# Kernel tuning notes

Measured on AMD Instinct MI355X. Metric: run time of the kernel, lower is better.

Reference implementation:

```python
import jax, jax.numpy as jnp
import numpy as np
import math

STAGE_NUM = 5
EPS = 1e-6

def _l2norm(a, axis):
    return a / (EPS + jnp.linalg.norm(a, axis=axis, keepdims=True))

def setup_inputs() -> dict:
    key = jax.random.key(0)
    k1, k2, k3, k4 = jax.random.split(key, 4)
    b, n, c, h, w, k, out_c = 4, 4, 256, 64, 64, 128, 256
    x = jax.random.normal(k1, (b, c, h, w), dtype=jnp.float32)
    querys = jax.random.normal(k2, (b * n, c, h, w), dtype=jnp.float32)
    # mu init: normal(0, sqrt(2/k)) then l2norm over channel dim
    mu0 = jax.random.normal(k3, (1, c, k), dtype=jnp.float32) * math.sqrt(2.0 / k)
    mu0 = _l2norm(mu0, axis=1)
    # conv weight: normal(0, sqrt(2/(kh*kw*out_c)))
    fan = 3 * 3 * out_c
    conv_w = jax.random.normal(k4, (out_c, 2 * c, 3, 3), dtype=jnp.float32) * math.sqrt(2.0 / fan)
    conv_b = jnp.zeros((out_c,), dtype=jnp.float32)
    return {"x": x, "querys": querys, "mu0": mu0, "conv_w": conv_w, "conv_b": conv_b, "n": n}

def reference(x, querys, mu0, conv_w, conv_b, n):
    b, c, h, w = x.shape
    k = mu0.shape[2]
    xf = x.reshape(b, c, h * w)                       # [b, c, L]
    mu = jnp.broadcast_to(mu0, (b, c, k))

    # EM iterations (torch.no_grad -> stop_gradient)
    def em_step(mu, _):
        z = jnp.einsum('bcl,bck->blk', xf, mu)        # [b, L, k]
        z = jax.nn.softmax(z, axis=2)
        z_ = z / (EPS + jnp.sum(z, axis=1, keepdims=True))
        mu = jnp.einsum('bcl,blk->bck', xf, z_)       # [b, c, k]
        mu = _l2norm(mu, axis=1)
        return mu, None
    mu, _ = jax.lax.scan(em_step, mu, None, length=STAGE_NUM)
    mu = jax.lax.stop_gradient(mu)

    org_query = querys                                 # [b*n, c, h, w]
    q = querys.reshape(b, n, c, h, w).transpose(0, 2, 1, 3, 4).reshape(b, c, n * h * w)
    q_z = jax.nn.softmax(jnp.einsum('bcl,bck->blk', q, mu), axis=2)  # [b, nL, k]
    q_z = jax.lax.stop_gradient(q_z)

    rec = jnp.einsum('bck,blk->bcl', mu, q_z)          # [b, c, n*h*w]
    rec = rec.reshape(b, c, n, h, w).transpose(0, 2, 1, 3, 4).reshape(b * n, c, h, w)

    cat = jnp.concatenate((org_query, rec), axis=1)    # [b*n, 2c, h, w]
    out = jax.lax.conv_general_dilated(
        cat, conv_w, window_strides=(1, 1), padding='SAME',
        dimension_numbers=('NCHW', 'OIHW', 'NCHW'))
    out = out + conv_b[None, :, None, None]
    return (out, mu)
```

## Files before the change

### kernel.cpp

```cpp
#include <hip/hip_runtime.h>
#include <hip/hip_bf16.h>

#define B   4
#define NN  4
#define C   256
#define HH  64
#define WW  64
#define L   4096
#define NL  16384
#define K   128
#define OC  256
#define IC2 512
#define EPSV 1e-6f
#define PW  66
#define PA  4356

typedef __hip_bfloat16 bf16;
typedef __attribute__((ext_vector_type(8))) __bf16 bf16x8;
typedef __attribute__((ext_vector_type(4))) float f32x4;

#define AS1(p) ((const __attribute__((address_space(1))) void*)(p))
#define AS3(p) ((__attribute__((address_space(3))) void*)(p))

__global__ void k_init(const float* __restrict__ mu0, float* __restrict__ mu_f,
                       bf16* __restrict__ mub) {
    int i = blockIdx.x * 256 + threadIdx.x;
    int rem = i & 32767;
    int k = rem >> 8, c = rem & 255;
    float v = mu0[c * 128 + k];
    mu_f[i] = v;
    mub[i]  = __float2bfloat16(v);
}

__global__ void k_prepx(const float* __restrict__ x, bf16* __restrict__ xb,
                        bf16* __restrict__ xt) {
    __shared__ float ld[64][65];
    int lt = blockIdx.x, ct = blockIdx.y, b = blockIdx.z;
    int t = threadIdx.x;
    #pragma unroll
    for (int i = 0; i < 16; i++) {
        int idx = t + i * 256;
        int ch = idx >> 6, xl = idx & 63;
        size_t a = ((size_t)b * C + ct * 64 + ch) * L + lt * 64 + xl;
        float v = x[a];
        ld[ch][xl] = v;
        xb[a] = __float2bfloat16(v);
    }
    __syncthreads();
    #pragma unroll
    for (int i = 0; i < 16; i++) {
        int idx = t + i * 256;
        int xl = idx >> 6, ch = idx & 63;
        xt[((size_t)b * L + lt * 64 + xl) * 256 + ct * 64 + ch] = __float2bfloat16(ld[ch][xl]);
    }
}

__global__ void k_prepq(const float* __restrict__ qy, bf16* __restrict__ P2) {
    __shared__ float ld[64][65];
    int y = blockIdx.x, ct = blockIdx.y, img = blockIdx.z;
    int t = threadIdx.x;
    #pragma unroll
    for (int i = 0; i < 16; i++) {
        int idx = t + i * 256;
        int ch = idx >> 6, xl = idx & 63;
        ld[ch][xl] = qy[((size_t)img * C + ct * 64 + ch) * L + y * WW + xl];
    }
    __syncthreads();
    #pragma unroll
    for (int i = 0; i < 16; i++) {
        int idx = t + i * 256;
        int xl = idx >> 6, ch = idx & 63;
        P2[((size_t)img * PA + (size_t)(y + 1) * PW + xl + 1) * 512 + ct * 64 + ch] =
            __float2bfloat16(ld[ch][xl]);
    }
}

__global__ void k_zborder(uint4* __restrict__ P2) {
    int pi = blockIdx.x, img = blockIdx.y, t = threadIdx.x;
    int y, x;
    if      (pi < 66)  { y = 0;        x = pi; }
    else if (pi < 132) { y = 65;       x = pi - 66; }
    else if (pi < 196) { y = pi - 131; x = 0; }
    else               { y = pi - 195; x = 65; }
    P2[((size_t)img * PA + (size_t)y * PW + x) * 64 + t] = uint4{0, 0, 0, 0};
}

__global__ void k_wprep(const float* __restrict__ cw, bf16* __restrict__ wb) {
    int idx = blockIdx.x * 256 + threadIdx.x;
    if (idx >= 9 * OC * IC2) return;
    int r  = idx / (OC * IC2);
    int oc = (idx / IC2) & 255;
    int ic = idx & 511;
    wb[idx] = __float2bfloat16(cw[((size_t)oc * IC2 + ic) * 9 + r]);
}

__global__ void __launch_bounds__(256) k_z(const bf16* __restrict__ xt,
                                           const bf16* __restrict__ mub,
                                           bf16* __restrict__ zt) {
    __shared__ __align__(16) char smem[12288];
    char* tA = smem;
    char* tB = smem + 8192;
    int t = threadIdx.x, w = t >> 6, lane = t & 63;
    int b = blockIdx.y, l0 = blockIdx.x * 64;
    const bf16* Ab = mub + (size_t)b * K * C;
    const bf16* Bb = xt + ((size_t)b * L + l0) * C;
    int srow = t >> 2, sseg = t & 3, aseg = sseg ^ (srow & 3);
    char* dA0 = tA + w * 1024;
    char* dA1 = tA + 4096 + w * 1024;
    char* dB  = tB + w * 1024;
    int aoff[8], boff;
    #pragma unroll
    for (int i = 0; i < 8; i++) {
        int rowA = i * 16 + (lane & 15);
        aoff[i] = rowA * 64 + (((lane >> 4) ^ (rowA & 3)) << 4);
    }
    { int rowB = w * 16 + (lane & 15);
      boff = rowB * 64 + (((lane >> 4) ^ (rowB & 3)) << 4); }
    f32x4 acc[8];
    #pragma unroll
    for (int i = 0; i < 8; i++) acc[i] = f32x4{0.f, 0.f, 0.f, 0.f};
    for (int s = 0; s < 8; s++) {
        int cb0 = s * 32 + aseg * 8;
        __syncthreads();
        __builtin_amdgcn_global_load_lds(AS1(Ab + (size_t)srow * C + cb0),        AS3(dA0), 16, 0, 0);
        __builtin_amdgcn_global_load_lds(AS1(Ab + (size_t)(srow + 64) * C + cb0), AS3(dA1), 16, 0, 0);
        __builtin_amdgcn_global_load_lds(AS1(Bb + (size_t)srow * C + cb0),        AS3(dB),  16, 0, 0);
        __syncthreads();
        bf16x8 bfr = *(bf16x8*)(tB + boff);
        #pragma unroll
        for (int i = 0; i < 8; i++) {
            bf16x8 af = *(bf16x8*)(tA + aoff[i]);
            acc[i] = __builtin_amdgcn_mfma_f32_16x16x32_bf16(af, bfr, acc[i], 0, 0, 0);
        }
    }
    float m = -1e30f;
    #pragma unroll
    for (int i = 0; i < 8; i++)
        #pragma unroll
        for (int r = 0; r < 4; r++) m = fmaxf(m, acc[i][r]);
    m = fmaxf(m, __shfl_xor(m, 16, 64));
    m = fmaxf(m, __shfl_xor(m, 32, 64));
    float ssum = 0.f;
    #pragma unroll
    for (int i = 0; i < 8; i++)
        #pragma unroll
        for (int r = 0; r < 4; r++) { acc[i][r] = __expf(acc[i][r] - m); ssum += acc[i][r]; }
    ssum += __shfl_xor(ssum, 16, 64);
    ssum += __shfl_xor(ssum, 32, 64);
    float inv = 1.f / ssum;
    int quad = lane >> 4, col = lane & 15;
    bf16* zb = zt + (size_t)b * K * L + l0 + w * 16 + col;
    #pragma unroll
    for (int i = 0; i < 8; i++)
        #pragma unroll
        for (int r = 0; r < 4; r++) {
            int k = i * 16 + quad * 4 + r;
            zb[(size_t)k * L] = __float2bfloat16(acc[i][r] * inv);
        }
}

__global__ void __launch_bounds__(256) k_mu(const bf16* __restrict__ zt,
                                            const bf16* __restrict__ xb,
                                            float* __restrict__ part) {
    __shared__ __align__(16) char smem[12288];
    char* tA = smem;
    char* tB = smem + 8192;
    int t = threadIdx.x, w = t >> 6, lane = t & 63;
    int ct = blockIdx.x, chunk = blockIdx.y, b = blockIdx.z;
    const bf16* Ab = zt + (size_t)b * K * L + chunk * 256;
    const bf16* Bb = xb + ((size_t)b * C + ct * 64) * L + chunk * 256;
    int srow = t >> 2, sseg = t & 3, aseg = sseg ^ (srow & 3);
    char* dA0 = tA + w * 1024; char* dA1 = tA + 4096 + w * 1024;
    char* dB0 = tB + w * 1024;
    int wm = w >> 1, wn = w & 1;
    int aoff[4], boff[2];
    #pragma unroll
    for (int i = 0; i < 4; i++) {
        int rowA = wm * 64 + i * 16 + (lane & 15);
        aoff[i] = rowA * 64 + (((lane >> 4) ^ (rowA & 3)) << 4);
    }
    #pragma unroll
    for (int j = 0; j < 2; j++) {
        int rowB = wn * 32 + j * 16 + (lane & 15);
        boff[j] = rowB * 64 + (((lane >> 4) ^ (rowB & 3)) << 4);
    }
    f32x4 acc[4][2];
    #pragma unroll
    for (int i = 0; i < 4; i++)
        #pragma unroll
        for (int j = 0; j < 2; j++) acc[i][j] = f32x4{0.f, 0.f, 0.f, 0.f};
    for (int s = 0; s < 8; s++) {
        int lb = s * 32 + aseg * 8;
        __syncthreads();
        __builtin_amdgcn_global_load_lds(AS1(Ab + (size_t)srow * L + lb),        AS3(dA0), 16, 0, 0);
        __builtin_amdgcn_global_load_lds(AS1(Ab + (size_t)(srow + 64) * L + lb), AS3(dA1), 16, 0, 0);
        __builtin_amdgcn_global_load_lds(AS1(Bb + (size_t)srow * L + lb),        AS3(dB0), 16, 0, 0);
        __syncthreads();
        bf16x8 af[4], bfr[2];
        #pragma unroll
        for (int i = 0; i < 4; i++) af[i]  = *(bf16x8*)(tA + aoff[i]);
        #pragma unroll
        for (int j = 0; j < 2; j++) bfr[j] = *(bf16x8*)(tB + boff[j]);
        #pragma unroll
        for (int i = 0; i < 4; i++)
            #pragma unroll
            for (int j = 0; j < 2; j++)
                acc[i][j] = __builtin_amdgcn_mfma_f32_16x16x32_bf16(af[i], bfr[j], acc[i][j], 0, 0, 0);
    }
    float* pb = part + ((size_t)(b * 16 + chunk) * K) * C + ct * 64;
    int quad = lane >> 4, col = lane & 15;
    #pragma unroll
    for (int i = 0; i < 4; i++) {
        int k = wm * 64 + i * 16 + quad * 4;
        #pragma unroll
        for (int j = 0; j < 2; j++) {
            int c = wn * 32 + j * 16 + col;
            #pragma unroll
            for (int r = 0; r < 4; r++)
                pb[(size_t)(k + r) * C + c] = acc[i][j][r];
        }
    }
}

__global__ void k_norm(const float* __restrict__ part, float* __restrict__ mu_f,
                       bf16* __restrict__ mub, bf16* __restrict__ muT) {
    int b = blockIdx.x >> 7, k = blockIdx.x & 127, lane = threadIdx.x;
    float v[4] = {0.f, 0.f, 0.f, 0.f};
    for (int ch = 0; ch < 16; ch++) {
        const float* p = part + ((size_t)(b * 16 + ch) * K + k) * C;
        #pragma unroll
        for (int j = 0; j < 4; j++) v[j] += p[lane + j * 64];
    }
    float s = v[0]*v[0] + v[1]*v[1] + v[2]*v[2] + v[3]*v[3];
    for (int o = 32; o > 0; o >>= 1) s += __shfl_xor(s, o, 64);
    float r = 1.f / (EPSV + sqrtf(s));
    float* mf = mu_f + ((size_t)b * K + k) * C;
    bf16*  mb = mub  + ((size_t)b * K + k) * C;
    bf16*  mt = muT  + (size_t)b * C * K + k;
    #pragma unroll
    for (int j = 0; j < 4; j++) {
        float val = v[j] * r;
        int c = lane + j * 64;
        mf[c] = val;
        mb[c] = __float2bfloat16(val);
        mt[(size_t)c * K] = __float2bfloat16(val);
    }
}

__global__ void __launch_bounds__(256) k_qzrec(const bf16* __restrict__ P2r,
                                               const bf16* __restrict__ mub,
                                               const bf16* __restrict__ muT,
                                               bf16* __restrict__ P2w) {
    __shared__ __align__(16) char smem[46080];
    char* tA = smem;
    char* tB = smem + 4096;
    char* zl = smem + 12288;
    char* mt = smem + 29696;
    int t = threadIdx.x, w = t >> 6, lane = t & 63;
    int b = blockIdx.y, tile = blockIdx.x;
    int n = tile >> 6, y = tile & 63;
    int img = b * NN + n;
    const bf16* Ab = P2r + ((size_t)img * PA + (size_t)(y + 1) * PW + 1) * 512;
    const bf16* Bb = mub + (size_t)b * K * C;
    int srow = t >> 2, sseg = t & 3, aseg = sseg ^ (srow & 3);
    char* dA  = tA + w * 1024;
    char* dB0 = tB + w * 1024;
    char* dB1 = tB + 4096 + w * 1024;
    int q = lane >> 4, col = lane & 15;
    int boff[8], aoff;
    #pragma unroll
    for (int j = 0; j < 8; j++) {
        int rowB = j * 16 + col;
        boff[j] = rowB * 64 + ((q ^ (rowB & 3)) << 4);
    }
    { int rowA = w * 16 + col;
      aoff = rowA * 64 + ((q ^ (rowA & 3)) << 4); }
    f32x4 acc[8];
    #pragma unroll
    for (int j = 0; j < 8; j++) acc[j] = f32x4{0.f, 0.f, 0.f, 0.f};
    for (int s = 0; s < 8; s++) {
        int cb0 = s * 32 + aseg * 8;
        __syncthreads();
        __builtin_amdgcn_global_load_lds(AS1(Ab + (size_t)srow * 512 + cb0),      AS3(dA),  16, 0, 0);
        __builtin_amdgcn_global_load_lds(AS1(Bb + (size_t)srow * C + cb0),        AS3(dB0), 16, 0, 0);
        __builtin_amdgcn_global_load_lds(AS1(Bb + (size_t)(srow + 64) * C + cb0), AS3(dB1), 16, 0, 0);
        __syncthreads();
        bf16x8 af = *(bf16x8*)(tA + aoff);
        #pragma unroll
        for (int j = 0; j < 8; j++) {
            bf16x8 bfr = *(bf16x8*)(tB + boff[j]);
            acc[j] = __builtin_amdgcn_mfma_f32_16x16x32_bf16(af, bfr, acc[j], 0, 0, 0);
        }
    }
    #pragma unroll
    for (int r = 0; r < 4; r++) {
        float mm = acc[0][r];
        #pragma unroll
        for (int j = 1; j < 8; j++) mm = fmaxf(mm, acc[j][r]);
        mm = fmaxf(mm, __shfl_xor(mm, 1, 64));
        mm = fmaxf(mm, __shfl_xor(mm, 2, 64));
        mm = fmaxf(mm, __shfl_xor(mm, 4, 64));
        mm = fmaxf(mm, __shfl_xor(mm, 8, 64));
        float ss = 0.f;
        float e[8];
        #pragma unroll
        for (int j = 0; j < 8; j++) { e[j] = __expf(acc[j][r] - mm); ss += e[j]; }
        ss += __shfl_xor(ss, 1, 64);
        ss += __shfl_xor(ss, 2, 64);
        ss += __shfl_xor(ss, 4, 64);
        ss += __shfl_xor(ss, 8, 64);
        float inv = 1.f / ss;
        int zrow = w * 16 + q * 4 + r;
        #pragma unroll
        for (int j = 0; j < 8; j++)
            *(bf16*)(zl + zrow * 272 + (j * 16 + col) * 2) = __float2bfloat16(e[j] * inv);
    }
    const bf16* Mb = muT + (size_t)b * C * K;
    int mrow = (lane >> 2);
    int mseg = lane & 3;
    #pragma unroll
    for (int it2 = 0; it2 < 4; it2++) {
        int row = w * 64 + it2 * 16 + mrow;
        int sg = mseg ^ ((row ^ (row >> 2)) & 3);
        __builtin_amdgcn_global_load_lds(AS1(Mb + (size_t)row * K + sg * 8),
            AS3(mt + (w * 64 + it2 * 16) * 64), 16, 0, 0);
    }
    __syncthreads();
    bf16x8 afz[4];
    #pragma unroll
    for (int ch = 0; ch < 4; ch++)
        afz[ch] = *(bf16x8*)(zl + (w * 16 + col) * 272 + ch * 64 + q * 16);
    f32x4 acc2[16];
    #pragma unroll
    for (int j = 0; j < 16; j++) acc2[j] = f32x4{0.f, 0.f, 0.f, 0.f};
    for (int s = 0; s < 4; s++) {
        #pragma unroll
        for (int j = 0; j < 16; j++) {
            int rr = j * 16 + col;
            bf16x8 bm = *(bf16x8*)(mt + rr * 64 + ((q ^ ((rr ^ (rr >> 2)) & 3)) << 4));
            acc2[j] = __builtin_amdgcn_mfma_f32_16x16x32_bf16(afz[s], bm, acc2[j], 0, 0, 0);
        }
        if (s < 3) {
            __syncthreads();
            #pragma unroll
            for (int it2 = 0; it2 < 4; it2++) {
                int row = w * 64 + it2 * 16 + mrow;
                int sg = mseg ^ ((row ^ (row >> 2)) & 3);
                __builtin_amdgcn_global_load_lds(AS1(Mb + (size_t)row * K + (s + 1) * 32 + sg * 8),
                    AS3(mt + (w * 64 + it2 * 16) * 64), 16, 0, 0);
            }
            __syncthreads();
        }
    }
    #pragma unroll
    for (int r = 0; r < 4; r++) {
        int xg = w * 16 + q * 4 + r;
        bf16* dst = P2w + ((size_t)img * PA + (size_t)(y + 1) * PW + xg + 1) * 512 + 256;
        #pragma unroll
        for (int j = 0; j < 16; j++)
            dst[j * 16 + col] = __float2bfloat16(acc2[j][r]);
    }
}

__global__ void __launch_bounds__(256, 2) k_conv(const bf16* __restrict__ P2,
                                                 const bf16* __restrict__ Wb,
                                                 const float* __restrict__ cb,
                                                 float* __restrict__ out) {
    __shared__ __align__(16) char smem[49920];
    char* inl = smem;
    char* wld = smem + 25344;
    int t = threadIdx.x, w = t >> 6, lane = t & 63;
    int m0  = blockIdx.x * 128;
    int y0  = blockIdx.y * 4;
    int img = blockIdx.z;
    int srow = t >> 2;
    int aseg = (t & 3) ^ ((srow ^ (srow >> 2)) & 3);
    int wm = w >> 1, wn = w & 1;
    int q = lane >> 4, lane15 = lane & 15;

    int aoff[4];
    #pragma unroll
    for (int i = 0; i < 4; i++) {
        int rowA = wm * 64 + i * 16 + lane15;
        aoff[i] = rowA * 64 + (((q ^ (rowA ^ (rowA >> 2))) & 3) << 4);
    }

    auto stageIN = [&](int cc) {
        size_t ibase = (size_t)img * PA * 512 + cc * 32;
        #pragma unroll
        for (int it = 0; it < 6; it++) {
            unsigned g = it * 256 + t;
            unsigned row = g / 264u, ps = g - row * 264u;
            unsigned px = ps >> 2, s0 = ps & 3;
            unsigned sg = s0 ^ ((px ^ (px >> 1)) & 3);
            __builtin_amdgcn_global_load_lds(
                AS1(P2 + ibase + ((size_t)(y0 + row) * PW + px) * 512 + sg * 8),
                AS3(inl + it * 4096 + w * 1024), 16, 0, 0);
        }
        if (t < 48) {
            unsigned g = 1536 + t;
            unsigned row = g / 264u, ps = g - row * 264u;
            unsigned px = ps >> 2, s0 = ps & 3;
            unsigned sg = s0 ^ ((px ^ (px >> 1)) & 3);
            __builtin_amdgcn_global_load_lds(
                AS1(P2 + ibase + ((size_t)(y0 + row) * PW + px) * 512 + sg * 8),
                AS3(inl + 24576), 16, 0, 0);
        }
    };

    f32x4 acc[4][8];
    #pragma unroll
    for (int i = 0; i < 4; i++) {
        int oc = m0 + wm * 64 + i * 16 + q * 4;
        #pragma unroll
        for (int r = 0; r < 4; r++) {
            float bv = cb[oc + r];
            #pragma unroll
            for (int j = 0; j < 8; j++) acc[i][j][r] = bv;
        }
    }

    stageIN(0);
    {
        const bf16* w0 = Wb + (size_t)(m0 + srow) * IC2 + aseg * 8;
        __builtin_amdgcn_global_load_lds(AS1(w0),                         AS3(wld + w * 1024), 16, 0, 0);
        __builtin_amdgcn_global_load_lds(AS1(w0 + (size_t)64 * IC2),      AS3(wld + 4096 + w * 1024), 16, 0, 0);
        const bf16* w1 = w0 + (size_t)(OC * IC2);
        __builtin_amdgcn_global_load_lds(AS1(w1),                         AS3(wld + 8192 + w * 1024), 16, 0, 0);
        __builtin_amdgcn_global_load_lds(AS1(w1 + (size_t)64 * IC2),      AS3(wld + 8192 + 4096 + w * 1024), 16, 0, 0);
    }
    asm volatile("s_waitcnt vmcnt(0)" ::: "memory");
    __builtin_amdgcn_s_barrier();
    asm volatile("" ::: "memory");

    for (int cc = 0; cc < 16; cc++) {
        #pragma unroll
        for (int rt = 0; rt < 9; rt++) {
            const int dy = rt / 3, dx = rt % 3;
            char* wbuf = wld + (rt % 3) * 8192;
            bf16x8 af[4];
            #pragma unroll
            for (int i = 0; i < 4; i++) af[i] = *(bf16x8*)(wbuf + aoff[i]);
            const bool doPf = (cc * 9 + rt + 2) < 144;
            if (doPf) {
                const int g2 = rt + 2;
                const int rt2 = (g2 >= 9) ? g2 - 9 : g2;
                const int cc2 = cc + (g2 >= 9 ? 1 : 0);
                char* wdst = wld + ((rt + 2) % 3) * 8192;
                const bf16* wsrc = Wb + (size_t)rt2 * (OC * IC2) + (size_t)(m0 + srow) * IC2
                                 + cc2 * 32 + aseg * 8;
                __builtin_amdgcn_global_load_lds(AS1(wsrc),                    AS3(wdst + w * 1024), 16, 0, 0);
                __builtin_amdgcn_global_load_lds(AS1(wsrc + (size_t)64 * IC2), AS3(wdst + 4096 + w * 1024), 16, 0, 0);
            }
            __builtin_amdgcn_s_setprio(1);
            #pragma unroll
            for (int j = 0; j < 8; j++) {
                int p = (j & 3) * 16 + lane15 + dx;
                int rowsel = 2 * wn + (j >> 2) + dy;
                bf16x8 bfr = *(bf16x8*)(inl + rowsel * 4224 + p * 64 +
                                        (((q ^ (p ^ (p >> 1))) & 3) << 4));
                #pragma unroll
                for (int i = 0; i < 4; i++)
                    acc[i][j] = __builtin_amdgcn_mfma_f32_16x16x32_bf16(af[i], bfr, acc[i][j], 0, 0, 0);
            }
            __builtin_amdgcn_s_setprio(0);
            if (rt == 8) {
                if (cc < 15) {
                    asm volatile("" ::: "memory");
                    __builtin_amdgcn_s_barrier();
                    asm volatile("" ::: "memory");
                    stageIN(cc + 1);
                    asm volatile("s_waitcnt vmcnt(0)" ::: "memory");
                    __builtin_amdgcn_s_barrier();
                    asm volatile("" ::: "memory");
                }
            } else {
                if (doPf) asm volatile("s_waitcnt vmcnt(2)" ::: "memory");
                else      asm volatile("s_waitcnt vmcnt(0)" ::: "memory");
                __builtin_amdgcn_s_barrier();
                asm volatile("" ::: "memory");
            }
        }
    }

    #pragma unroll
    for (int i = 0; i < 4; i++) {
        int oc = m0 + wm * 64 + i * 16 + q * 4;
        #pragma unroll
        for (int j = 0; j < 8; j++) {
            int px = blockIdx.y * 256 + wn * 128 + (j >> 2) * 64 + (j & 3) * 16 + lane15;
            #pragma unroll
            for (int r = 0; r < 4; r++)
                out[((size_t)img * OC + oc + r) * L + px] = acc[i][j][r];
        }
    }
}

__global__ void k_muout(const float* __restrict__ mu_f, float* __restrict__ out) {
    int i = blockIdx.x * 256 + threadIdx.x;
    int b = i >> 15, rem = i & 32767;
    int c = rem >> 7, k = rem & 127;
    out[(size_t)16777216 + i] = mu_f[((size_t)b * K + k) * C + c];
}

extern "C" void kernel_launch(void* const* d_in, const int* in_sizes, int n_in,
                              void* d_out, int out_size, void* d_ws, size_t ws_size,
                              hipStream_t stream) {
    const float* x   = (const float*)d_in[0];
    const float* qy  = (const float*)d_in[1];
    const float* mu0 = (const float*)d_in[2];
    const float* cw  = (const float*)d_in[3];
    const float* cb  = (const float*)d_in[4];
    float* out = (float*)d_out;

    char* ws = (char*)d_ws;
    float* mu_f = (float*)(ws);
    bf16*  mu_b = (bf16*) (ws + 524288);
    bf16*  muT  = (bf16*) (ws + 786432);
    bf16*  Wb   = (bf16*) (ws + 1048576);
    bf16*  zt   = (bf16*) (ws + 3407872);
    bf16*  P2   = (bf16*) (ws + 20185088);
    bf16*  x_bf = (bf16*) (ws + 20185088);
    float* part = (float*)(ws + 20185088 + 8388608);
    bf16*  xt   = (bf16*) (ws + 20185088 + 16777216);

    k_init<<<512, 256, 0, stream>>>(mu0, mu_f, mu_b);
    k_prepx<<<dim3(64, 4, 4), 256, 0, stream>>>(x, x_bf, xt);

    for (int it = 0; it < 5; it++) {
        k_z<<<dim3(64, 4), 256, 0, stream>>>(xt, mu_b, zt);
        k_mu<<<dim3(4, 16, 4), 256, 0, stream>>>(zt, x_bf, part);
        k_norm<<<512, 64, 0, stream>>>(part, mu_f, mu_b, muT);
    }

    k_prepq<<<dim3(64, 4, 16), 256, 0, stream>>>(qy, P2);
    k_zborder<<<dim3(260, 16), 64, 0, stream>>>((uint4*)P2);
    k_wprep<<<4608, 256, 0, stream>>>(cw, Wb);

    k_qzrec<<<dim3(256, 4), 256, 0, stream>>>(P2, mu_b, muT, P2);
    k_conv<<<dim3(2, 16, 16), 256, 0, stream>>>(P2, Wb, cb, out);
    k_muout<<<512, 256, 0, stream>>>(mu_f, out);
}
```

Measured before the change: 405.3 us.

## Merge prep kernels, write mu output from norm, double-buffer muT staging in qzrec

```diff
diff --git a/kernel.cpp b/kernel.cpp
--- a/kernel.cpp
+++ b/kernel.cpp
@@ -22,14 +22,11 @@
 #define AS1(p) ((const __attribute__((address_space(1))) void*)(p))
 #define AS3(p) ((__attribute__((address_space(3))) void*)(p))
 
-__global__ void k_init(const float* __restrict__ mu0, float* __restrict__ mu_f,
-                       bf16* __restrict__ mub) {
+__global__ void k_init(const float* __restrict__ mu0, bf16* __restrict__ mub) {
     int i = blockIdx.x * 256 + threadIdx.x;
     int rem = i & 32767;
     int k = rem >> 8, c = rem & 255;
-    float v = mu0[c * 128 + k];
-    mu_f[i] = v;
-    mub[i]  = __float2bfloat16(v);
+    mub[i] = __float2bfloat16(mu0[c * 128 + k]);
 }
 
 __global__ void k_prepx(const float* __restrict__ x, bf16* __restrict__ xb,
@@ -55,43 +52,43 @@
     }
 }
 
-__global__ void k_prepq(const float* __restrict__ qy, bf16* __restrict__ P2) {
+__global__ void k_mid(const float* __restrict__ qy, bf16* __restrict__ P2,
+                      const float* __restrict__ cw, bf16* __restrict__ wb) {
     __shared__ float ld[64][65];
-    int y = blockIdx.x, ct = blockIdx.y, img = blockIdx.z;
-    int t = threadIdx.x;
-    #pragma unroll
-    for (int i = 0; i < 16; i++) {
-        int idx = t + i * 256;
-        int ch = idx >> 6, xl = idx & 63;
-        ld[ch][xl] = qy[((size_t)img * C + ct * 64 + ch) * L + y * WW + xl];
-    }
-    __syncthreads();
-    #pragma unroll
-    for (int i = 0; i < 16; i++) {
-        int idx = t + i * 256;
-        int xl = idx >> 6, ch = idx & 63;
-        P2[((size_t)img * PA + (size_t)(y + 1) * PW + xl + 1) * 512 + ct * 64 + ch] =
-            __float2bfloat16(ld[ch][xl]);
-    }
-}
-
-__global__ void k_zborder(uint4* __restrict__ P2) {
-    int pi = blockIdx.x, img = blockIdx.y, t = threadIdx.x;
-    int y, x;
-    if      (pi < 66)  { y = 0;        x = pi; }
-    else if (pi < 132) { y = 65;       x = pi - 66; }
-    else if (pi < 196) { y = pi - 131; x = 0; }
-    else               { y = pi - 195; x = 65; }
-    P2[((size_t)img * PA + (size_t)y * PW + x) * 64 + t] = uint4{0, 0, 0, 0};
-}
-
-__global__ void k_wprep(const float* __restrict__ cw, bf16* __restrict__ wb) {
-    int idx = blockIdx.x * 256 + threadIdx.x;
-    if (idx >= 9 * OC * IC2) return;
-    int r  = idx / (OC * IC2);
-    int oc = (idx / IC2) & 255;
-    int ic = idx & 511;
-    wb[idx] = __float2bfloat16(cw[((size_t)oc * IC2 + ic) * 9 + r]);
+    int bid = blockIdx.x, t = threadIdx.x;
+    if (bid < 4096) {
+        int y = bid & 63, ct = (bid >> 6) & 3, img = bid >> 8;
+        #pragma unroll
+        for (int i = 0; i < 16; i++) {
+            int idx = t + i * 256;
+            int ch = idx >> 6, xl = idx & 63;
+            ld[ch][xl] = qy[((size_t)img * C + ct * 64 + ch) * L + y * WW + xl];
+        }
+        __syncthreads();
+        #pragma unroll
+        for (int i = 0; i < 16; i++) {
+            int idx = t + i * 256;
+            int xl = idx >> 6, ch = idx & 63;
+            P2[((size_t)img * PA + (size_t)(y + 1) * PW + xl + 1) * 512 + ct * 64 + ch] =
+                __float2bfloat16(ld[ch][xl]);
+        }
+    } else if (bid < 5136) {
+        int zi = bid - 4096;
+        int img = zi / 65, grp = zi - img * 65;
+        int pi = grp * 4 + (t >> 6), tt = t & 63;
+        int y, x;
+        if      (pi < 66)  { y = 0;        x = pi; }
+        else if (pi < 132) { y = 65;       x = pi - 66; }
+        else if (pi < 196) { y = pi - 131; x = 0; }
+        else               { y = pi - 195; x = 65; }
+        ((uint4*)P2)[((size_t)img * PA + (size_t)y * PW + x) * 64 + tt] = uint4{0, 0, 0, 0};
+    } else {
+        int idx = (bid - 5136) * 256 + t;
+        int r  = idx / (OC * IC2);
+        int oc = (idx / IC2) & 255;
+        int ic = idx & 511;
+        wb[idx] = __float2bfloat16(cw[((size_t)oc * IC2 + ic) * 9 + r]);
+    }
 }
 
 __global__ void __launch_bounds__(256) k_z(const bf16* __restrict__ xt,
@@ -222,8 +219,8 @@
     }
 }
 
-__global__ void k_norm(const float* __restrict__ part, float* __restrict__ mu_f,
-                       bf16* __restrict__ mub, bf16* __restrict__ muT) {
+__global__ void k_norm(const float* __restrict__ part, bf16* __restrict__ mub,
+                       bf16* __restrict__ muT, float* __restrict__ outT, int last) {
     int b = blockIdx.x >> 7, k = blockIdx.x & 127, lane = threadIdx.x;
     float v[4] = {0.f, 0.f, 0.f, 0.f};
     for (int ch = 0; ch < 16; ch++) {
@@ -234,16 +231,15 @@
     float s = v[0]*v[0] + v[1]*v[1] + v[2]*v[2] + v[3]*v[3];
     for (int o = 32; o > 0; o >>= 1) s += __shfl_xor(s, o, 64);
     float r = 1.f / (EPSV + sqrtf(s));
-    float* mf = mu_f + ((size_t)b * K + k) * C;
-    bf16*  mb = mub  + ((size_t)b * K + k) * C;
-    bf16*  mt = muT  + (size_t)b * C * K + k;
+    bf16*  mb = mub + ((size_t)b * K + k) * C;
+    bf16*  mt = muT + (size_t)b * C * K + k;
     #pragma unroll
     for (int j = 0; j < 4; j++) {
         float val = v[j] * r;
         int c = lane + j * 64;
-        mf[c] = val;
         mb[c] = __float2bfloat16(val);
         mt[(size_t)c * K] = __float2bfloat16(val);
+        if (last) outT[(size_t)b * 32768 + (size_t)c * 128 + k] = val;
     }
 }
 
@@ -316,16 +312,20 @@
             *(bf16*)(zl + zrow * 272 + (j * 16 + col) * 2) = __float2bfloat16(e[j] * inv);
     }
     const bf16* Mb = muT + (size_t)b * C * K;
-    int mrow = (lane >> 2);
-    int mseg = lane & 3;
-    #pragma unroll
-    for (int it2 = 0; it2 < 4; it2++) {
-        int row = w * 64 + it2 * 16 + mrow;
-        int sg = mseg ^ ((row ^ (row >> 2)) & 3);
-        __builtin_amdgcn_global_load_lds(AS1(Mb + (size_t)row * K + sg * 8),
-            AS3(mt + (w * 64 + it2 * 16) * 64), 16, 0, 0);
-    }
-    __syncthreads();
+    auto stageMT = [&](int p) {
+        int s = p >> 1, h = p & 1;
+        #pragma unroll
+        for (int it2 = 0; it2 < 2; it2++) {
+            int u = it2 * 256 + t;
+            int row = u >> 2, seg = u & 3;
+            int grow = h * 128 + row;
+            int sg = seg ^ ((grow ^ (grow >> 2)) & 3);
+            __builtin_amdgcn_global_load_lds(AS1(Mb + (size_t)grow * K + s * 32 + sg * 8),
+                AS3(mt + h * 8192 + it2 * 4096 + w * 1024), 16, 0, 0);
+        }
+    };
+    stageMT(0);
+    stageMT(1);
     bf16x8 afz[4];
     #pragma unroll
     for (int ch = 0; ch < 4; ch++)
@@ -333,24 +333,26 @@
     f32x4 acc2[16];
     #pragma unroll
     for (int j = 0; j < 16; j++) acc2[j] = f32x4{0.f, 0.f, 0.f, 0.f};
-    for (int s = 0; s < 4; s++) {
-        #pragma unroll
-        for (int j = 0; j < 16; j++) {
+    #pragma unroll
+    for (int p = 0; p < 8; p++) {
+        if (p < 7) asm volatile("s_waitcnt vmcnt(2)" ::: "memory");
+        else       asm volatile("s_waitcnt vmcnt(0)" ::: "memory");
+        __builtin_amdgcn_s_barrier();
+        asm volatile("" ::: "memory");
+        const int s = p >> 1, h = p & 1;
+        #pragma unroll
+        for (int jj = 0; jj < 8; jj++) {
+            int j = h * 8 + jj;
             int rr = j * 16 + col;
-            bf16x8 bm = *(bf16x8*)(mt + rr * 64 + ((q ^ ((rr ^ (rr >> 2)) & 3)) << 4));
+            int local = rr - h * 128;
+            bf16x8 bm = *(bf16x8*)(mt + h * 8192 + local * 64 +
+                                   ((q ^ ((rr ^ (rr >> 2)) & 3)) << 4));
             acc2[j] = __builtin_amdgcn_mfma_f32_16x16x32_bf16(afz[s], bm, acc2[j], 0, 0, 0);
         }
-        if (s < 3) {
-            __syncthreads();
-            #pragma unroll
-            for (int it2 = 0; it2 < 4; it2++) {
-                int row = w * 64 + it2 * 16 + mrow;
-                int sg = mseg ^ ((row ^ (row >> 2)) & 3);
-                __builtin_amdgcn_global_load_lds(AS1(Mb + (size_t)row * K + (s + 1) * 32 + sg * 8),
-                    AS3(mt + (w * 64 + it2 * 16) * 64), 16, 0, 0);
-            }
-            __syncthreads();
-        }
+        asm volatile("" ::: "memory");
+        __builtin_amdgcn_s_barrier();
+        asm volatile("" ::: "memory");
+        if (p < 6) stageMT(p + 2);
     }
     #pragma unroll
     for (int r = 0; r < 4; r++) {
@@ -496,13 +498,6 @@
     }
 }
 
-__global__ void k_muout(const float* __restrict__ mu_f, float* __restrict__ out) {
-    int i = blockIdx.x * 256 + threadIdx.x;
-    int b = i >> 15, rem = i & 32767;
-    int c = rem >> 7, k = rem & 127;
-    out[(size_t)16777216 + i] = mu_f[((size_t)b * K + k) * C + c];
-}
-
 extern "C" void kernel_launch(void* const* d_in, const int* in_sizes, int n_in,
                               void* d_out, int out_size, void* d_ws, size_t ws_size,
                               hipStream_t stream) {
@@ -514,7 +509,6 @@
     float* out = (float*)d_out;
 
     char* ws = (char*)d_ws;
-    float* mu_f = (float*)(ws);
     bf16*  mu_b = (bf16*) (ws + 524288);
     bf16*  muT  = (bf16*) (ws + 786432);
     bf16*  Wb   = (bf16*) (ws + 1048576);
@@ -524,20 +518,17 @@
     float* part = (float*)(ws + 20185088 + 8388608);
     bf16*  xt   = (bf16*) (ws + 20185088 + 16777216);
 
-    k_init<<<512, 256, 0, stream>>>(mu0, mu_f, mu_b);
+    k_init<<<512, 256, 0, stream>>>(mu0, mu_b);
     k_prepx<<<dim3(64, 4, 4), 256, 0, stream>>>(x, x_bf, xt);
 
     for (int it = 0; it < 5; it++) {
         k_z<<<dim3(64, 4), 256, 0, stream>>>(xt, mu_b, zt);
         k_mu<<<dim3(4, 16, 4), 256, 0, stream>>>(zt, x_bf, part);
-        k_norm<<<512, 64, 0, stream>>>(part, mu_f, mu_b, muT);
-    }
-
-    k_prepq<<<dim3(64, 4, 16), 256, 0, stream>>>(qy, P2);
-    k_zborder<<<dim3(260, 16), 64, 0, stream>>>((uint4*)P2);
-    k_wprep<<<4608, 256, 0, stream>>>(cw, Wb);
+        k_norm<<<512, 64, 0, stream>>>(part, mu_b, muT, out + 16777216, it == 4 ? 1 : 0);
+    }
+
+    k_mid<<<9744, 256, 0, stream>>>(qy, P2, cw, Wb);
 
     k_qzrec<<<dim3(256, 4), 256, 0, stream>>>(P2, mu_b, muT, P2);
     k_conv<<<dim3(2, 16, 16), 256, 0, stream>>>(P2, Wb, cb, out);
-    k_muout<<<512, 256, 0, stream>>>(mu_f, out);
-}
+}
```

After: 393.9 us. 1.03x faster.
